# Kernel optimization log

Measured on AMD Instinct MI355X. Metric: run time of the kernel, lower is better.

## Reference

```python
import jax, jax.numpy as jnp
import numpy as np

DIM = 1024
HEADS = 16
HEAD_DIM = DIM // HEADS
HIDDEN = 4096  # mlp_ratio * dim
SCALE = HEAD_DIM ** -0.5
LN_EPS = 1e-5


def softmax_one(x):
    # softmax with +1 in the denominator (after max subtraction), per source
    m = jnp.max(x, axis=-1, keepdims=True)
    e = jnp.exp(x - m)
    return e / (1.0 + jnp.sum(e, axis=-1, keepdims=True))


def layer_norm(x, g, b):
    mu = jnp.mean(x, axis=-1, keepdims=True)
    var = jnp.mean(jnp.square(x - mu), axis=-1, keepdims=True)
    return (x - mu) * jax.lax.rsqrt(var + LN_EPS) * g + b


def setup_inputs() -> dict:
    key = jax.random.key(0)
    ks = jax.random.split(key, 12)
    B, C, N = 2, DIM, 2048
    x = jax.random.normal(ks[0], (B, C, N), dtype=jnp.float32)
    mask = jax.random.randint(ks[1], (B, HEADS, N), 0, 2, dtype=jnp.int32)
    s = 0.02
    return {
        'x': x,
        'mask': mask,
        'qkv_w': jax.random.normal(ks[2], (3 * DIM, DIM), jnp.float32) * s,
        'qkv_b': jnp.zeros((3 * DIM,), jnp.float32),
        'proj_w': jax.random.normal(ks[3], (DIM, DIM), jnp.float32) * s,
        'proj_b': jnp.zeros((DIM,), jnp.float32),
        'fc1_w': jax.random.normal(ks[4], (HIDDEN, DIM), jnp.float32) * s,
        'fc1_b': jnp.zeros((HIDDEN,), jnp.float32),
        'ln_g': jnp.ones((HIDDEN,), jnp.float32),
        'ln_b': jnp.zeros((HIDDEN,), jnp.float32),
        'fc2_w': jax.random.normal(ks[5], (DIM, HIDDEN), jnp.float32) * s,
        'fc2_b': jnp.zeros((DIM,), jnp.float32),
    }


def reference(x, mask, qkv_w, qkv_b, proj_w, proj_b, fc1_w, fc1_b, ln_g, ln_b, fc2_w, fc2_b):
    B, C, N = x.shape
    xt = jnp.swapaxes(x, 1, 2)  # (B, N, C)

    # ----- attention -----
    qkv = xt @ qkv_w.T + qkv_b                      # (B, N, 3C)
    qkv = qkv.reshape(B, N, 3, HEADS, HEAD_DIM)
    qkv = jnp.transpose(qkv, (2, 0, 3, 1, 4))       # (3, B, H, N, Dh)
    q, k, v = qkv[0], qkv[1], qkv[2]
    scores = jnp.einsum('bhnd,bhmd->bhnm', q * SCALE, k)  # (B, H, N, N)
    scores = jnp.where(mask[:, :, :, None] == 0, -1e9, scores)
    attn = softmax_one(scores)
    out = jnp.einsum('bhnm,bhmd->bhnd', attn, v)    # (B, H, N, Dh)
    # faithful to source: permute(0,3,1,2).reshape(B,N,C) -> scrambled merge
    out = jnp.transpose(out, (0, 3, 1, 2)).reshape(B, N, C)
    out = out @ proj_w.T + proj_b

    # faithful residual: attn_out + ls1(attn_out) with ls1 = Identity
    h = out + out                                   # (B, N, C)

    # ----- MLP (timm Mlp: fc1 -> GELU -> LayerNorm -> fc2) -----
    m = h @ fc1_w.T + fc1_b
    m = jax.nn.gelu(m, approximate=False)
    m = layer_norm(m, ln_g, ln_b)
    m = m @ fc2_w.T + fc2_b
    y = h + m                                       # (B, N, C)

    return jnp.swapaxes(y, 1, 2)                    # (B, C, N)
```

## Files before the change

kernel.cpp:

```cpp
#include <hip/hip_runtime.h>
#include <math.h>

#define DIMC   1024
#define NTOK   2048
#define BATCH  2
#define HEADS  16
#define HDIM   64
#define HIDDEN 4096
#define MROWS  (BATCH*NTOK)
#define QSZ    ((size_t)BATCH*HEADS*NTOK*HDIM)
#define QSC    0.18033688f

typedef unsigned short ushort_t;
typedef __attribute__((ext_vector_type(8))) short short8;
typedef __attribute__((ext_vector_type(4))) float f32x4;
typedef __attribute__((ext_vector_type(4))) unsigned short us4;

__device__ __forceinline__ ushort_t f2b(float f) {
  union { float f; unsigned int u; } cv; cv.f = f;
  unsigned int u = cv.u;
  unsigned int r = (u + 0x7fffu + ((u >> 16) & 1u)) >> 16;
  return (ushort_t)r;
}

__device__ __forceinline__ float b2f(ushort_t b) {
  union { unsigned int u; float f; } cv; cv.u = ((unsigned int)b) << 16;
  return cv.f;
}

__device__ __forceinline__ float fexp2(float x) {
#if __has_builtin(__builtin_amdgcn_exp2f)
  return __builtin_amdgcn_exp2f(x);
#else
  return exp2f(x);
#endif
}

__device__ __forceinline__ void gl_lds16(const void* g, void* l) {
  __builtin_amdgcn_global_load_lds(
      (const __attribute__((address_space(1))) void*)g,
      (__attribute__((address_space(3))) void*)l, 16, 0, 0);
}

__global__ __launch_bounds__(256) void k_pre(const float* __restrict__ x,
                                             const float* __restrict__ w0,
                                             const float* __restrict__ w1,
                                             const float* __restrict__ w2,
                                             const float* __restrict__ w3,
                                             ushort_t* __restrict__ xt,
                                             ushort_t* __restrict__ o0,
                                             ushort_t* __restrict__ o1,
                                             ushort_t* __restrict__ o2,
                                             ushort_t* __restrict__ o3) {
  __shared__ float t[32][33];
  int bid = blockIdx.x;
  if (bid < 4096) {
    int b   = bid >> 11;
    int rem = bid & 2047;
    int n0  = (rem & 63) * 32;
    int c0  = (rem >> 6) * 32;
    int tx = threadIdx.x & 31, ty = threadIdx.x >> 5;
#pragma unroll
    for (int l = 0; l < 4; l++)
      t[ty + l * 8][tx] = x[((size_t)(b * DIMC + c0 + ty + l * 8)) * NTOK + n0 + tx];
    __syncthreads();
#pragma unroll
    for (int l = 0; l < 4; l++)
      xt[((size_t)(b * NTOK + n0 + ty + l * 8)) * DIMC + c0 + tx] = f2b(t[tx][ty + l * 8]);
  } else {
    int cb = bid - 4096;
    const float* in; ushort_t* out; int base;
    if (cb < 3072)      { in = w0; out = o0; base = cb; }
    else if (cb < 4096) { in = w1; out = o1; base = cb - 3072; }
    else if (cb < 8192) { in = w2; out = o2; base = cb - 4096; }
    else                { in = w3; out = o3; base = cb - 8192; }
    int i = base * 256 + threadIdx.x;
    float4 v = ((const float4*)in)[i];
    us4 o; o.x = f2b(v.x); o.y = f2b(v.y); o.z = f2b(v.z); o.w = f2b(v.w);
    ((us4*)out)[i] = o;
  }
}

template <int EPI, int NTX8, int KSTRIDE, int KLEN, int XROW>
__global__ __launch_bounds__(256) void k_gemm_bf16(const ushort_t* __restrict__ A,
                                                   const ushort_t* __restrict__ W,
                                                   const float* __restrict__ bias,
                                                   void* __restrict__ outv) {
  __shared__ ushort_t As[2][128 * 32];
  __shared__ ushort_t Bs[2][128 * 32];
  const int tid = threadIdx.x;
  const int lane = tid & 63, wv = tid >> 6;
  const int bid = blockIdx.x, kz = blockIdx.y;
  const int xcd = bid & 7, t = bid >> 3;
  const int row0 = XROW ? (xcd * NTX8 + (t % NTX8)) * 128 : (t / NTX8) * 128;
  const int col0 = XROW ? (t / NTX8) * 128 : (xcd * NTX8 + (t % NTX8)) * 128;
  const int wrow0 = (wv >> 1) * 64, wcol0 = (wv & 1) * 64;
  const int lm = lane & 15, lq = lane >> 4;
  const int srow = wv * 32 + (lane >> 2);
  const int gch = (lane & 3) ^ ((lane >> 3) & 3);
  const int sw8 = (lq ^ ((lm >> 1) & 3)) * 8;

  const ushort_t* Ab = A + (size_t)(row0 + srow) * KSTRIDE + (size_t)kz * KLEN + gch * 8;
  const ushort_t* Wb = W + (size_t)(col0 + srow) * KSTRIDE + (size_t)kz * KLEN + gch * 8;
  const size_t rstep = (size_t)16 * KSTRIDE;

  f32x4 acc[4][4];
#pragma unroll
  for (int i = 0; i < 4; i++)
#pragma unroll
    for (int j = 0; j < 4; j++) acc[i][j] = (f32x4){0.f, 0.f, 0.f, 0.f};

#define STAGE(buf, k0) do {                                      \
    gl_lds16(Ab + (k0),         &As[buf][wv * 1024]);            \
    gl_lds16(Ab + rstep + (k0), &As[buf][wv * 1024 + 512]);      \
    gl_lds16(Wb + (k0),         &Bs[buf][wv * 1024]);            \
    gl_lds16(Wb + rstep + (k0), &Bs[buf][wv * 1024 + 512]);      \
  } while (0)

  auto compute = [&](int buf) {
    short8 af[4], bf[4];
#pragma unroll
    for (int mi = 0; mi < 4; mi++)
      af[mi] = *(const short8*)&As[buf][(wrow0 + mi * 16 + lm) * 32 + sw8];
#pragma unroll
    for (int ni = 0; ni < 4; ni++)
      bf[ni] = *(const short8*)&Bs[buf][(wcol0 + ni * 16 + lm) * 32 + sw8];
#pragma unroll
    for (int mi = 0; mi < 4; mi++)
#pragma unroll
      for (int ni = 0; ni < 4; ni++)
        acc[mi][ni] = __builtin_amdgcn_mfma_f32_16x16x32_bf16(af[mi], bf[ni], acc[mi][ni], 0, 0, 0);
  };

  constexpr int S = KLEN / 32;
  STAGE(0, 0);
#pragma unroll 1
  for (int kk = 0; kk < S; kk++) {
    __syncthreads();
    if (kk + 1 < S) STAGE((kk + 1) & 1, (kk + 1) * 32);
    compute(kk & 1);
  }
#undef STAGE

#pragma unroll
  for (int mi = 0; mi < 4; mi++) {
#pragma unroll
    for (int ni = 0; ni < 4; ni++) {
#pragma unroll
      for (int r = 0; r < 4; r++) {
        const int row = row0 + wrow0 + mi * 16 + lq * 4 + r;
        const int col = col0 + wcol0 + ni * 16 + lm;
        float v = acc[mi][ni][r];
        if (EPI != 4) v += bias[col];
        if (EPI == 0) {
          int which = col >> 10, rem = col & 1023, hh = rem >> 6, d = rem & 63;
          int bb = row >> 11, n = row & 2047;
          size_t bh = (size_t)(bb * HEADS + hh);
          ushort_t* o16 = (ushort_t*)outv;
          if (which == 0)
            o16[(bh * NTOK + n) * HDIM + d] = f2b(v * QSC);
          else if (which == 1)
            o16[QSZ + (bh * NTOK + n) * HDIM + d] = f2b(v);
          else
            o16[2 * QSZ + (bh * HDIM + d) * NTOK + n] = f2b(v);
        } else {
          ((ushort_t*)outv)[(size_t)kz * MROWS * DIMC + (size_t)row * DIMC + col] = f2b(v);
        }
      }
    }
  }
}

__global__ __launch_bounds__(512, 2) void k_gemm256_fc1(const ushort_t* __restrict__ A,
                                                        const ushort_t* __restrict__ W,
                                                        const float* __restrict__ bias,
                                                        ushort_t* __restrict__ out) {
  __shared__ ushort_t As[2][256 * 64];
  __shared__ ushort_t Bs[2][256 * 64];
  const int tid = threadIdx.x;
  const int lane = tid & 63, wid = tid >> 6;
  const int wr = wid >> 2, wc = wid & 3;
  const int lm = lane & 15, quad = lane >> 4;
  const int bid = blockIdx.x;
  const int lin = (bid & 7) * 32 + (bid >> 3);
  const int row0 = (lin >> 4) * 256, col0 = (lin & 15) * 256;
  const int swz = lm & 7;

  const int gch = (tid & 7) ^ ((tid >> 3) & 7);
  const ushort_t* Ab = A + (size_t)(row0 + (tid >> 3)) * 1024 + gch * 8;
  const ushort_t* Wb = W + (size_t)(col0 + (tid >> 3)) * 1024 + gch * 8;
  const int dbase = wid * 512;

  auto stA = [&](int buf, int half, int kt) {
    const ushort_t* s = Ab + (size_t)(half * 128) * 1024 + kt * 64;
    gl_lds16(s,             &As[buf][half * 8192 + dbase]);
    gl_lds16(s + 64 * 1024, &As[buf][half * 8192 + 4096 + dbase]);
  };
  auto stB = [&](int buf, int half, int kt) {
    const ushort_t* s = Wb + (size_t)(half * 128) * 1024 + kt * 64;
    gl_lds16(s,             &Bs[buf][half * 8192 + dbase]);
    gl_lds16(s + 64 * 1024, &Bs[buf][half * 8192 + 4096 + dbase]);
  };

  f32x4 acc[8][4];
#pragma unroll
  for (int i = 0; i < 8; i++)
#pragma unroll
    for (int j = 0; j < 4; j++) acc[i][j] = (f32x4){0.f, 0.f, 0.f, 0.f};

  short8 af[4][2], bf[4][2];

  auto rdAf = [&](int buf, int mih) {
#pragma unroll
    for (int mi = 0; mi < 4; mi++)
#pragma unroll
      for (int ks = 0; ks < 2; ks++)
        af[mi][ks] = *(const short8*)&As[buf][(wr * 128 + (mih * 4 + mi) * 16 + lm) * 64 +
                                             (((ks * 4 + quad) ^ swz) * 8)];
  };
  auto rdBf = [&](int buf, int nh) {
#pragma unroll
    for (int nn = 0; nn < 2; nn++)
#pragma unroll
      for (int ks = 0; ks < 2; ks++)
        bf[nh * 2 + nn][ks] = *(const short8*)&Bs[buf][(wc * 64 + (nh * 2 + nn) * 16 + lm) * 64 +
                                                       (((ks * 4 + quad) ^ swz) * 8)];
  };
  auto quadMM = [&](int m0, int n0) {
    __builtin_amdgcn_s_setprio(1);
#pragma unroll
    for (int mi = 0; mi < 4; mi++)
#pragma unroll
      for (int ni = 0; ni < 2; ni++)
#pragma unroll
        for (int ks = 0; ks < 2; ks++)
          acc[m0 + mi][n0 + ni] = __builtin_amdgcn_mfma_f32_16x16x32_bf16(
              af[mi][ks], bf[n0 + ni][ks], acc[m0 + mi][n0 + ni], 0, 0, 0);
    __builtin_amdgcn_s_setprio(0);
  };

  constexpr int NT = 16;
  stB(0, 0, 0); stB(0, 1, 0);
  stA(0, 0, 0); stA(0, 1, 0);
  stB(1, 0, 1); stB(1, 1, 1);

#pragma unroll 1
  for (int kt = 0; kt < NT; kt++) {
    const int buf = kt & 1;
    if (kt + 1 < NT) __builtin_amdgcn_s_waitcnt(0x0F74);
    else             __builtin_amdgcn_s_waitcnt(0x0F70);
    __builtin_amdgcn_s_barrier();
    asm volatile("" ::: "memory");

    rdAf(buf, 0);
    rdBf(buf, 0);
    if (kt + 1 < NT) stA(buf ^ 1, 0, kt + 1);
    asm volatile("" ::: "memory");
    __builtin_amdgcn_s_barrier();
    quadMM(0, 0);
    __builtin_amdgcn_s_barrier();
    asm volatile("" ::: "memory");

    rdBf(buf, 1);
    if (kt + 1 < NT) stA(buf ^ 1, 1, kt + 1);
    asm volatile("" ::: "memory");
    __builtin_amdgcn_s_barrier();
    quadMM(0, 2);
    __builtin_amdgcn_s_barrier();
    asm volatile("" ::: "memory");

    rdAf(buf, 1);
    if (kt + 2 < NT) stB(buf, 0, kt + 2);
    asm volatile("" ::: "memory");
    __builtin_amdgcn_s_barrier();
    quadMM(4, 2);
    __builtin_amdgcn_s_barrier();
    asm volatile("" ::: "memory");

    if (kt + 2 < NT) stB(buf, 1, kt + 2);
    asm volatile("" ::: "memory");
    __builtin_amdgcn_s_barrier();
    quadMM(4, 0);
  }

#pragma unroll
  for (int mi = 0; mi < 8; mi++)
#pragma unroll
    for (int ni = 0; ni < 4; ni++)
#pragma unroll
      for (int r = 0; r < 4; r++) {
        const int row = row0 + wr * 128 + mi * 16 + quad * 4 + r;
        const int col = col0 + wc * 64 + ni * 16 + lm;
        out[(size_t)row * HIDDEN + col] = f2b(acc[mi][ni][r] + bias[col]);
      }
}

__global__ __launch_bounds__(256) void k_comb_proj(const ushort_t* __restrict__ p0,
                                                   const ushort_t* __restrict__ p1,
                                                   const float* __restrict__ bias,
                                                   ushort_t* __restrict__ hb) {
  int i = blockIdx.x * 256 + threadIdx.x;
  int colb = (i & 255) * 4;
  us4 a = ((const us4*)p0)[i];
  us4 b = ((const us4*)p1)[i];
  us4 o;
  o.x = f2b(2.f * (b2f(a.x) + b2f(b.x) + bias[colb + 0]));
  o.y = f2b(2.f * (b2f(a.y) + b2f(b.y) + bias[colb + 1]));
  o.z = f2b(2.f * (b2f(a.z) + b2f(b.z) + bias[colb + 2]));
  o.w = f2b(2.f * (b2f(a.w) + b2f(b.w) + bias[colb + 3]));
  ((us4*)hb)[i] = o;
}

__global__ __launch_bounds__(256) void k_comb_fc2(const ushort_t* __restrict__ p0,
                                                  const ushort_t* __restrict__ p1,
                                                  const ushort_t* __restrict__ hb,
                                                  const float* __restrict__ bias,
                                                  float* __restrict__ out) {
  __shared__ float t[32][33];
  int b  = blockIdx.z;
  int c0 = blockIdx.y * 32, n0 = blockIdx.x * 32;
  int tx = threadIdx.x, ty = threadIdx.y;
#pragma unroll
  for (int l = 0; l < 4; l++) {
    size_t idx = ((size_t)(b * NTOK + n0 + ty + l * 8)) * DIMC + c0 + tx;
    t[ty + l * 8][tx] = b2f(p0[idx]) + b2f(p1[idx]) + b2f(hb[idx]) + bias[c0 + tx];
  }
  __syncthreads();
#pragma unroll
  for (int l = 0; l < 4; l++)
    out[((size_t)(b * DIMC + c0 + ty + l * 8)) * NTOK + n0 + tx] = t[tx][ty + l * 8];
}

__global__ __launch_bounds__(256) void k_attn_mfma(const ushort_t* __restrict__ qkv,
                                                   const int* __restrict__ mask,
                                                   ushort_t* __restrict__ scram) {
  __shared__ ushort_t Kl[2][64 * 64];
  __shared__ ushort_t Vl[2][64 * 64];
  __shared__ ushort_t Pl[4 * 32 * 72];
  const int tid = threadIdx.x;
  const int lane = tid & 63, w = tid >> 6;
  const int lm = lane & 15, quad = lane >> 4;
  const int bh = blockIdx.y, b = bh >> 4, h = bh & 15;
  const int q0 = blockIdx.x * 128 + w * 32;
  const ushort_t* qg  = qkv + (size_t)bh * NTOK * HDIM;
  const ushort_t* kg  = qkv + QSZ + (size_t)bh * NTOK * HDIM;
  const ushort_t* vTg = qkv + 2 * QSZ + (size_t)bh * HDIM * NTOK;
  ushort_t* Pw = &Pl[w * 32 * 72];

  const short8 ones = {0x3F80, 0x3F80, 0x3F80, 0x3F80, 0x3F80, 0x3F80, 0x3F80, 0x3F80};

  short8 qf[2][2];
#pragma unroll
  for (int qs = 0; qs < 2; qs++)
#pragma unroll
    for (int hf = 0; hf < 2; hf++)
      qf[qs][hf] = *(const short8*)&qg[(size_t)(q0 + qs * 16 + lm) * HDIM + hf * 32 + quad * 8];

  bool mk[2][4];
#pragma unroll
  for (int qs = 0; qs < 2; qs++)
#pragma unroll
    for (int r = 0; r < 4; r++)
      mk[qs][r] = mask[(size_t)bh * NTOK + q0 + qs * 16 + quad * 4 + r] != 0;

  f32x4 O[2][4], La[2];
#pragma unroll
  for (int qs = 0; qs < 2; qs++) {
    La[qs] = (f32x4){0.f, 0.f, 0.f, 0.f};
#pragma unroll
    for (int r = 0; r < 4; r++) O[qs][r] = (f32x4){0.f, 0.f, 0.f, 0.f};
  }

  const int s0 = tid, s1 = tid + 256;
  const int r0 = s0 >> 3, g0 = (s0 & 7) ^ (r0 & 7);
  const int r1 = s1 >> 3, g1 = (s1 & 7) ^ (r1 & 7);

  gl_lds16(kg + (size_t)r0 * HDIM + g0 * 8, &Kl[0][s0 * 8]);
  gl_lds16(kg + (size_t)r1 * HDIM + g1 * 8, &Kl[0][s1 * 8]);
  gl_lds16(vTg + (size_t)r0 * NTOK + g0 * 8, &Vl[0][s0 * 8]);
  gl_lds16(vTg + (size_t)r1 * NTOK + g1 * 8, &Vl[0][s1 * 8]);

  for (int kt = 0; kt < NTOK; kt += 64) {
    const int cur = (kt >> 6) & 1, nxt = cur ^ 1;
    __syncthreads();
    if (kt + 64 < NTOK) {
      gl_lds16(kg + (size_t)(kt + 64 + r0) * HDIM + g0 * 8, &Kl[nxt][s0 * 8]);
      gl_lds16(kg + (size_t)(kt + 64 + r1) * HDIM + g1 * 8, &Kl[nxt][s1 * 8]);
      gl_lds16(vTg + (size_t)r0 * NTOK + kt + 64 + g0 * 8, &Vl[nxt][s0 * 8]);
      gl_lds16(vTg + (size_t)r1 * NTOK + kt + 64 + g1 * 8, &Vl[nxt][s1 * 8]);
    }

    short8 kf[4][2];
#pragma unroll
    for (int ksub = 0; ksub < 4; ksub++)
#pragma unroll
      for (int hf = 0; hf < 2; hf++)
        kf[ksub][hf] = *(const short8*)&Kl[cur][(ksub * 16 + lm) * 64 + ((4 * hf + quad) ^ (lm & 7)) * 8];

#pragma unroll
    for (int qs = 0; qs < 2; qs++) {
      f32x4 S[4];
#pragma unroll
      for (int ksub = 0; ksub < 4; ksub++) {
        S[ksub] = (f32x4){0.f, 0.f, 0.f, 0.f};
        S[ksub] = __builtin_amdgcn_mfma_f32_16x16x32_bf16(qf[qs][0], kf[ksub][0], S[ksub], 0, 0, 0);
        S[ksub] = __builtin_amdgcn_mfma_f32_16x16x32_bf16(qf[qs][1], kf[ksub][1], S[ksub], 0, 0, 0);
      }
#pragma unroll
      for (int r = 0; r < 4; r++) {
        const int prow = qs * 16 + quad * 4 + r;
#pragma unroll
        for (int ksub = 0; ksub < 4; ksub++) {
          float p = mk[qs][r] ? fexp2(S[ksub][r]) : 1.0f;
          Pw[prow * 72 + ksub * 16 + lm] = (ushort_t)(__float_as_uint(p) >> 16);
        }
      }
    }
    __builtin_amdgcn_s_waitcnt(0xC07F);

    short8 vf[4][2];
#pragma unroll
    for (int dsub = 0; dsub < 4; dsub++)
#pragma unroll
      for (int hf = 0; hf < 2; hf++)
        vf[dsub][hf] = *(const short8*)&Vl[cur][(dsub * 16 + lm) * 64 + ((4 * hf + quad) ^ (lm & 7)) * 8];

#pragma unroll
    for (int qs = 0; qs < 2; qs++) {
      short8 pf[2];
#pragma unroll
      for (int hf = 0; hf < 2; hf++)
        pf[hf] = *(const short8*)&Pw[(qs * 16 + lm) * 72 + hf * 32 + quad * 8];
#pragma unroll
      for (int dsub = 0; dsub < 4; dsub++) {
        O[qs][dsub] = __builtin_amdgcn_mfma_f32_16x16x32_bf16(pf[0], vf[dsub][0], O[qs][dsub], 0, 0, 0);
        O[qs][dsub] = __builtin_amdgcn_mfma_f32_16x16x32_bf16(pf[1], vf[dsub][1], O[qs][dsub], 0, 0, 0);
      }
      La[qs] = __builtin_amdgcn_mfma_f32_16x16x32_bf16(pf[0], ones, La[qs], 0, 0, 0);
      La[qs] = __builtin_amdgcn_mfma_f32_16x16x32_bf16(pf[1], ones, La[qs], 0, 0, 0);
    }
  }

#pragma unroll
  for (int qs = 0; qs < 2; qs++)
#pragma unroll
    for (int r = 0; r < 4; r++) {
      int n = q0 + qs * 16 + quad * 4 + r;
      float inv = 1.f / (1.f + La[qs][r]);
      int n1 = n >> 10, nn0 = n & 1023;
#pragma unroll
      for (int dsub = 0; dsub < 4; dsub++) {
        int d = dsub * 16 + lm;
        int np = d * 32 + h * 2 + n1;
        scram[((size_t)(b * NTOK + np)) * DIMC + nn0] = f2b(O[qs][dsub][r] * inv);
      }
    }
}

__global__ __launch_bounds__(256) void k_ln(ushort_t* __restrict__ mid,
                                            const float* __restrict__ g,
                                            const float* __restrict__ bta) {
  const int row = blockIdx.x;
  ushort_t* p = mid + (size_t)row * HIDDEN;
  const int tid = threadIdx.x;
  float lv[16];
  float s = 0.f, s2 = 0.f;
#pragma unroll
  for (int i = 0; i < 4; i++) {
    us4 u = *(const us4*)&p[tid * 4 + i * 1024];
#pragma unroll
    for (int j = 0; j < 4; j++) {
      float xx = b2f((j == 0) ? u.x : (j == 1) ? u.y : (j == 2) ? u.z : u.w);
      xx = 0.5f * xx * (1.f + erff(xx * 0.70710678118654752f));
      lv[i * 4 + j] = xx;
      s += xx;
      s2 += xx * xx;
    }
  }
#pragma unroll
  for (int off = 32; off > 0; off >>= 1) {
    s += __shfl_down(s, off);
    s2 += __shfl_down(s2, off);
  }
  __shared__ float rs[4], rs2[4];
  if ((tid & 63) == 0) { rs[tid >> 6] = s; rs2[tid >> 6] = s2; }
  __syncthreads();
  float ts = rs[0] + rs[1] + rs[2] + rs[3];
  float ts2 = rs2[0] + rs2[1] + rs2[2] + rs2[3];
  float mu = ts * (1.f / HIDDEN);
  float var = ts2 * (1.f / HIDDEN) - mu * mu;
  float rstd = rsqrtf(var + 1e-5f);
#pragma unroll
  for (int i = 0; i < 4; i++) {
    us4 o;
#pragma unroll
    for (int j = 0; j < 4; j++) {
      int f = tid * 4 + i * 1024 + j;
      float y = (lv[i * 4 + j] - mu) * rstd * g[f] + bta[f];
      ushort_t ob = f2b(y);
      if (j == 0) o.x = ob; else if (j == 1) o.y = ob; else if (j == 2) o.z = ob; else o.w = ob;
    }
    *(us4*)&p[tid * 4 + i * 1024] = o;
  }
}

extern "C" void kernel_launch(void* const* d_in, const int* in_sizes, int n_in,
                              void* d_out, int out_size, void* d_ws, size_t ws_size,
                              hipStream_t stream) {
  const float* x      = (const float*)d_in[0];
  const int*   mask   = (const int*)d_in[1];
  const float* qkv_w  = (const float*)d_in[2];
  const float* qkv_b  = (const float*)d_in[3];
  const float* proj_w = (const float*)d_in[4];
  const float* proj_b = (const float*)d_in[5];
  const float* fc1_w  = (const float*)d_in[6];
  const float* fc1_b  = (const float*)d_in[7];
  const float* ln_g   = (const float*)d_in[8];
  const float* ln_b   = (const float*)d_in[9];
  const float* fc2_w  = (const float*)d_in[10];
  const float* fc2_b  = (const float*)d_in[11];

  char* w = (char*)d_ws;
  ushort_t* qkv16  = (ushort_t*)w;           w += 3 * QSZ * 2;
  ushort_t* xtb    = (ushort_t*)w;           w += (size_t)MROWS * DIMC * 2;
  ushort_t* scramb = (ushort_t*)w;           w += (size_t)MROWS * DIMC * 2;
  ushort_t* hb     = (ushort_t*)w;           w += (size_t)MROWS * DIMC * 2;
  ushort_t* mid    = (ushort_t*)w;           w += (size_t)MROWS * HIDDEN * 2;
  ushort_t* wqkvb  = (ushort_t*)w;           w += (size_t)3 * DIMC * DIMC * 2;
  ushort_t* wprojb = (ushort_t*)w;           w += (size_t)DIMC * DIMC * 2;
  ushort_t* wfc1b  = (ushort_t*)w;           w += (size_t)HIDDEN * DIMC * 2;
  ushort_t* wfc2b  = (ushort_t*)w;           w += (size_t)DIMC * HIDDEN * 2;
  ushort_t* pbuf   = (ushort_t*)w;           w += (size_t)2 * MROWS * DIMC * 2;
  ushort_t* pbuf1  = pbuf + (size_t)MROWS * DIMC;

  k_pre<<<dim3(4096 + 12288), 256, 0, stream>>>(x, qkv_w, proj_w, fc1_w, fc2_w,
                                                xtb, wqkvb, wprojb, wfc1b, wfc2b);

  k_gemm_bf16<0, 4, DIMC, DIMC, 1><<<dim3(24 * 32), 256, 0, stream>>>(
      xtb, wqkvb, qkv_b, qkv16);
  k_attn_mfma<<<dim3(NTOK / 128, BATCH * HEADS), 256, 0, stream>>>(
      qkv16, mask, scramb);
  k_gemm_bf16<4, 4, DIMC, 512, 1><<<dim3(8 * 32, 2), 256, 0, stream>>>(
      scramb, wprojb, nullptr, pbuf);
  k_comb_proj<<<dim3(4096), 256, 0, stream>>>(pbuf, pbuf1, proj_b, hb);
  k_gemm256_fc1<<<dim3(256), 512, 0, stream>>>(hb, wfc1b, fc1_b, mid);
  k_ln<<<dim3(MROWS), 256, 0, stream>>>(mid, ln_g, ln_b);
  k_gemm_bf16<4, 4, HIDDEN, 2048, 1><<<dim3(8 * 32, 2), 256, 0, stream>>>(
      mid, wfc2b, nullptr, pbuf);
  k_comb_fc2<<<dim3(NTOK / 32, DIMC / 32, BATCH), dim3(32, 8), 0, stream>>>(
      pbuf, pbuf1, hb, fc2_b, (float*)d_out);
}
```

Before: 344.4 us.

## Template 256x256 GEMM and use it with split-K 4 for fc2

Generalizes the 256x256-tile fc1 GEMM kernel into a template with K stride, column-tile count and split-K index, then uses it for fc2 (K=4096 split into 4 slices of 1024) instead of the smaller-tile 2-way split-K kernel. The final combine kernel now sums four bf16 partial slices plus residual and bias. Larger tiles give more data reuse per block, at the cost of extra partial-buffer traffic and a 256-block grid that may underfill the GPU.

```diff
diff --git a/kernel.cpp b/kernel.cpp
--- a/kernel.cpp
+++ b/kernel.cpp
@@ -171,35 +171,36 @@
   }
 }
 
-__global__ __launch_bounds__(512, 2) void k_gemm256_fc1(const ushort_t* __restrict__ A,
-                                                        const ushort_t* __restrict__ W,
-                                                        const float* __restrict__ bias,
-                                                        ushort_t* __restrict__ out) {
+template <int EPI, int KSTRIDE, int NCT, int NB8>
+__global__ __launch_bounds__(512, 2) void k_gemm256(const ushort_t* __restrict__ A,
+                                                    const ushort_t* __restrict__ W,
+                                                    const float* __restrict__ bias,
+                                                    void* __restrict__ outv) {
   __shared__ ushort_t As[2][256 * 64];
   __shared__ ushort_t Bs[2][256 * 64];
   const int tid = threadIdx.x;
   const int lane = tid & 63, wid = tid >> 6;
   const int wr = wid >> 2, wc = wid & 3;
   const int lm = lane & 15, quad = lane >> 4;
-  const int bid = blockIdx.x;
-  const int lin = (bid & 7) * 32 + (bid >> 3);
-  const int row0 = (lin >> 4) * 256, col0 = (lin & 15) * 256;
+  const int bid = blockIdx.x, kz = blockIdx.y;
+  const int lin = (bid & 7) * NB8 + (bid >> 3);
+  const int row0 = (lin / NCT) * 256, col0 = (lin % NCT) * 256;
   const int swz = lm & 7;
 
   const int gch = (tid & 7) ^ ((tid >> 3) & 7);
-  const ushort_t* Ab = A + (size_t)(row0 + (tid >> 3)) * 1024 + gch * 8;
-  const ushort_t* Wb = W + (size_t)(col0 + (tid >> 3)) * 1024 + gch * 8;
+  const ushort_t* Ab = A + (size_t)(row0 + (tid >> 3)) * KSTRIDE + (size_t)kz * 1024 + gch * 8;
+  const ushort_t* Wb = W + (size_t)(col0 + (tid >> 3)) * KSTRIDE + (size_t)kz * 1024 + gch * 8;
   const int dbase = wid * 512;
 
   auto stA = [&](int buf, int half, int kt) {
-    const ushort_t* s = Ab + (size_t)(half * 128) * 1024 + kt * 64;
-    gl_lds16(s,             &As[buf][half * 8192 + dbase]);
-    gl_lds16(s + 64 * 1024, &As[buf][half * 8192 + 4096 + dbase]);
+    const ushort_t* s = Ab + (size_t)(half * 128) * KSTRIDE + kt * 64;
+    gl_lds16(s,                &As[buf][half * 8192 + dbase]);
+    gl_lds16(s + 64 * KSTRIDE, &As[buf][half * 8192 + 4096 + dbase]);
   };
   auto stB = [&](int buf, int half, int kt) {
-    const ushort_t* s = Wb + (size_t)(half * 128) * 1024 + kt * 64;
-    gl_lds16(s,             &Bs[buf][half * 8192 + dbase]);
-    gl_lds16(s + 64 * 1024, &Bs[buf][half * 8192 + 4096 + dbase]);
+    const ushort_t* s = Wb + (size_t)(half * 128) * KSTRIDE + kt * 64;
+    gl_lds16(s,                &Bs[buf][half * 8192 + dbase]);
+    gl_lds16(s + 64 * KSTRIDE, &Bs[buf][half * 8192 + 4096 + dbase]);
   };
 
   f32x4 acc[8][4];
@@ -291,7 +292,11 @@
       for (int r = 0; r < 4; r++) {
         const int row = row0 + wr * 128 + mi * 16 + quad * 4 + r;
         const int col = col0 + wc * 64 + ni * 16 + lm;
-        out[(size_t)row * HIDDEN + col] = f2b(acc[mi][ni][r] + bias[col]);
+        if (EPI == 2) {
+          ((ushort_t*)outv)[(size_t)row * HIDDEN + col] = f2b(acc[mi][ni][r] + bias[col]);
+        } else {
+          ((ushort_t*)outv)[(size_t)kz * MROWS * DIMC + (size_t)row * DIMC + col] = f2b(acc[mi][ni][r]);
+        }
       }
 }
 
@@ -311,19 +316,20 @@
   ((us4*)hb)[i] = o;
 }
 
-__global__ __launch_bounds__(256) void k_comb_fc2(const ushort_t* __restrict__ p0,
-                                                  const ushort_t* __restrict__ p1,
+__global__ __launch_bounds__(256) void k_comb_fc2(const ushort_t* __restrict__ p,
                                                   const ushort_t* __restrict__ hb,
                                                   const float* __restrict__ bias,
                                                   float* __restrict__ out) {
   __shared__ float t[32][33];
+  const size_t SL = (size_t)MROWS * DIMC;
   int b  = blockIdx.z;
   int c0 = blockIdx.y * 32, n0 = blockIdx.x * 32;
   int tx = threadIdx.x, ty = threadIdx.y;
 #pragma unroll
   for (int l = 0; l < 4; l++) {
     size_t idx = ((size_t)(b * NTOK + n0 + ty + l * 8)) * DIMC + c0 + tx;
-    t[ty + l * 8][tx] = b2f(p0[idx]) + b2f(p1[idx]) + b2f(hb[idx]) + bias[c0 + tx];
+    t[ty + l * 8][tx] = b2f(p[idx]) + b2f(p[idx + SL]) + b2f(p[idx + 2 * SL]) +
+                        b2f(p[idx + 3 * SL]) + b2f(hb[idx]) + bias[c0 + tx];
   }
   __syncthreads();
 #pragma unroll
@@ -530,7 +536,7 @@
   ushort_t* wprojb = (ushort_t*)w;           w += (size_t)DIMC * DIMC * 2;
   ushort_t* wfc1b  = (ushort_t*)w;           w += (size_t)HIDDEN * DIMC * 2;
   ushort_t* wfc2b  = (ushort_t*)w;           w += (size_t)DIMC * HIDDEN * 2;
-  ushort_t* pbuf   = (ushort_t*)w;           w += (size_t)2 * MROWS * DIMC * 2;
+  ushort_t* pbuf   = (ushort_t*)w;           w += (size_t)4 * MROWS * DIMC * 2;
   ushort_t* pbuf1  = pbuf + (size_t)MROWS * DIMC;
 
   k_pre<<<dim3(4096 + 12288), 256, 0, stream>>>(x, qkv_w, proj_w, fc1_w, fc2_w,
@@ -543,10 +549,9 @@
   k_gemm_bf16<4, 4, DIMC, 512, 1><<<dim3(8 * 32, 2), 256, 0, stream>>>(
       scramb, wprojb, nullptr, pbuf);
   k_comb_proj<<<dim3(4096), 256, 0, stream>>>(pbuf, pbuf1, proj_b, hb);
-  k_gemm256_fc1<<<dim3(256), 512, 0, stream>>>(hb, wfc1b, fc1_b, mid);
+  k_gemm256<2, 1024, 16, 32><<<dim3(256), 512, 0, stream>>>(hb, wfc1b, fc1_b, mid);
   k_ln<<<dim3(MROWS), 256, 0, stream>>>(mid, ln_g, ln_b);
-  k_gemm_bf16<4, 4, HIDDEN, 2048, 1><<<dim3(8 * 32, 2), 256, 0, stream>>>(
-      mid, wfc2b, nullptr, pbuf);
+  k_gemm256<4, 4096, 4, 8><<<dim3(64, 4), 512, 0, stream>>>(mid, wfc2b, nullptr, pbuf);
   k_comb_fc2<<<dim3(NTOK / 32, DIMC / 32, BATCH), dim3(32, 8), 0, stream>>>(
-      pbuf, pbuf1, hb, fc2_b, (float*)d_out);
-}
+      pbuf, hb, fc2_b, (float*)d_out);
+}
```

After: 337.0 us, median of 2. 1.02x faster.
